# Kernel tuning notes

Hardware: AMD Instinct MI355X
Metric: run time of the kernel (lower is better)

The kernel has to match this reference:

```python
import jax, jax.numpy as jnp
import numpy as np

N_HEAD = 16
N_KV = 4
HEAD_DIM = 64
QK_SCALE = 1.2
VE_GATE_CH = 12


def rms_norm(x):
    # F.rms_norm with default eps = finfo(dtype).eps, no learned scale
    eps = jnp.asarray(jnp.finfo(x.dtype).eps, x.dtype)
    return x * jax.lax.rsqrt(jnp.mean(x * x, axis=-1, keepdims=True) + eps)


def apply_rotary(x, cos, sin):
    # x: (B,T,H,D); cos/sin: (1,T,1,D//2)
    d = x.shape[-1] // 2
    x1, x2 = x[..., :d], x[..., d:]
    return jnp.concatenate([x1 * cos + x2 * sin, -x1 * sin + x2 * cos], axis=-1)


def setup_inputs() -> dict:
    key = jax.random.key(0)
    ks = jax.random.split(key, 8)
    B, T, C = 2, 2048, 1024
    x = jax.random.normal(ks[0], (B, T, C), jnp.float32)
    ve = jax.random.normal(ks[1], (B, T, N_KV * HEAD_DIM), jnp.float32)
    # realistic rotary tables for positions 0..T
    half = HEAD_DIM // 2
    inv_freq = 1.0 / (10000.0 ** (np.arange(half, dtype=np.float64) / half))
    ang = np.arange(T)[:, None] * inv_freq[None, :]
    cos = jnp.asarray(np.cos(ang), jnp.float32)[None, :, None, :]
    sin = jnp.asarray(np.sin(ang), jnp.float32)[None, :, None, :]
    s = 0.02
    Wq = jax.random.normal(ks[2], (N_HEAD * HEAD_DIM, C), jnp.float32) * s
    Wk = jax.random.normal(ks[3], (N_KV * HEAD_DIM, C), jnp.float32) * s
    Wv = jax.random.normal(ks[4], (N_KV * HEAD_DIM, C), jnp.float32) * s
    Wo = jax.random.normal(ks[5], (C, C), jnp.float32) * s
    Wg = jax.random.normal(ks[6], (N_KV, VE_GATE_CH), jnp.float32) * s
    return dict(x=x, ve=ve, cos=cos, sin=sin, Wq=Wq, Wk=Wk, Wv=Wv, Wo=Wo,
                Wg=Wg, window_left=1024)


def reference(x, ve, cos, sin, Wq, Wk, Wv, Wo, Wg, window_left):
    B, T, C = x.shape
    G = N_HEAD // N_KV  # GQA group size
    q = (x @ Wq.T).reshape(B, T, N_HEAD, HEAD_DIM)
    k = (x @ Wk.T).reshape(B, T, N_KV, HEAD_DIM)
    v = (x @ Wv.T).reshape(B, T, N_KV, HEAD_DIM)
    # sigmoid-gated value-embedding mixing
    gate = 3.0 * jax.nn.sigmoid(x[..., :VE_GATE_CH] @ Wg.T)  # (B,T,N_KV)
    v = v + gate[..., None] * ve.reshape(B, T, N_KV, HEAD_DIM)
    # RoPE -> RMSNorm -> qk_scale on both q and k
    q = rms_norm(apply_rotary(q, cos, sin)) * QK_SCALE
    k = rms_norm(apply_rotary(k, cos, sin)) * QK_SCALE
    # GQA attention with causal + sliding window (flash default scale 1/sqrt(d))
    qg = q.reshape(B, T, N_KV, G, HEAD_DIM)
    scale = 1.0 / jnp.sqrt(jnp.asarray(HEAD_DIM, q.dtype))
    scores = jnp.einsum('bqkgd,bskd->bkgqs', qg, k) * scale  # (B,N_KV,G,T,T)
    i = jnp.arange(T)[:, None]
    j = jnp.arange(T)[None, :]
    mask = (j <= i) & (i - j <= window_left)
    scores = jnp.where(mask, scores, jnp.asarray(-1e30, scores.dtype))
    attn = jax.nn.softmax(scores, axis=-1)
    y = jnp.einsum('bkgqs,bskd->bqkgd', attn, v).reshape(B, T, N_HEAD * HEAD_DIM)
    return y @ Wo.T
```

## Files before the change

### kernel.cpp

```cpp
#include <hip/hip_runtime.h>
#include <hip/hip_bf16.h>

#define B_ 2
#define T_ 2048
#define C_ 1024
#define NH 16
#define NKV 4
#define HD 64
#define NQKV 1536
#define KVB 64

typedef __attribute__((ext_vector_type(4))) float f32x4;
typedef __attribute__((ext_vector_type(8))) short bf16x8;
typedef __attribute__((ext_vector_type(4))) short bf16x4;

__device__ __forceinline__ unsigned short f2bf(float f) {
  __hip_bfloat16 h = __float2bfloat16(f);
  unsigned short u;
  __builtin_memcpy(&u, &h, 2);
  return u;
}

__device__ __forceinline__ void gload16(const void* g, void* l) {
  __builtin_amdgcn_global_load_lds(
      (const __attribute__((address_space(1))) void*)g,
      (__attribute__((address_space(3))) void*)l, 16, 0, 0);
}

__device__ __forceinline__ unsigned cvtpk(float lo, float hi_) {
  unsigned w;
  asm("v_cvt_pk_bf16_f32 %0, %1, %2" : "=v"(w) : "v"(lo), "v"(hi_));
  return w;
}

#define NX4  1048576
#define NW4  262144
#define NK4  65536
#define O1 (NX4)
#define O2 (O1 + NW4)
#define O3 (O2 + NK4)
#define O4 (O3 + NK4)
#define OT (O4 + NW4)

__global__ __launch_bounds__(256) void conv_all(
    const float* __restrict__ x, const float* __restrict__ wq, const float* __restrict__ wk,
    const float* __restrict__ wv, const float* __restrict__ wo,
    unsigned short* __restrict__ xb, unsigned short* __restrict__ wqkvb,
    unsigned short* __restrict__ wob) {
  int i = blockIdx.x * blockDim.x + threadIdx.x;
  const int stride = gridDim.x * blockDim.x;
  for (; i < OT; i += stride) {
    const float* src;
    unsigned short* dst;
    int j;
    if (i < O1)      { src = x;  dst = xb;                    j = i; }
    else if (i < O2) { src = wq; dst = wqkvb;                 j = i - O1; }
    else if (i < O3) { src = wk; dst = wqkvb + 1024 * 1024;   j = i - O2; }
    else if (i < O4) { src = wv; dst = wqkvb + 1280 * 1024;   j = i - O3; }
    else             { src = wo; dst = wob;                   j = i - O4; }
    const float4 v = reinterpret_cast<const float4*>(src)[j];
    ushort4 o;
    o.x = f2bf(v.x); o.y = f2bf(v.y); o.z = f2bf(v.z); o.w = f2bf(v.w);
    reinterpret_cast<ushort4*>(dst)[j] = o;
  }
}

#define BK 64

__global__ __launch_bounds__(256) void gemm_qkv(
    const unsigned short* __restrict__ A, const unsigned short* __restrict__ Bw,
    const float* __restrict__ x, const float* __restrict__ ve,
    const float* __restrict__ cosb, const float* __restrict__ sinb,
    const float* __restrict__ Wg,
    unsigned short* __restrict__ Qn, unsigned short* __restrict__ Kn,
    unsigned short* __restrict__ Vt) {
  constexpr int BMT = 128, MI = 4, NI = 2, K = 1024;
  __shared__ char smem[50176];
  unsigned short* AlB = (unsigned short*)smem;
  unsigned short* BlB = (unsigned short*)(smem + 32768);
  const int tid = threadIdx.x;
  const int lane = tid & 63;
  const int wid = tid >> 6;
  const int r = lane & 15, g = lane >> 4;
  const int wm = (wid >> 1) * 64, wn = (wid & 1) * 32;
  const int bm0 = blockIdx.y * BMT, bn0 = blockIdx.x * 64;
  const int lrow = lane >> 3;
  const int lcol = ((lane & 7) ^ lrow) * 8;
  const unsigned short* Asrc = A + (size_t)(bm0 + wid * 32 + lrow) * K + lcol;
  const unsigned short* Bsrc = Bw + (size_t)(bn0 + wid * 16 + lrow) * K + lcol;
  const int fsw = (r & 7) << 4;
  f32x4 acc[MI][NI] = {};

  auto stage = [&](int k0, int buf) {
#pragma unroll
    for (int i = 0; i < 4; ++i)
      gload16(Asrc + (size_t)(i * 8) * K + k0, AlB + buf * 8192 + (wid * 32 + i * 8) * BK);
#pragma unroll
    for (int i = 0; i < 2; ++i)
      gload16(Bsrc + (size_t)(i * 8) * K + k0, BlB + buf * 4096 + (wid * 16 + i * 8) * BK);
  };

  stage(0, 0);
  __syncthreads();
  const int nt = K / BK;
  for (int t = 0; t < nt; ++t) {
    const int cur = t & 1;
    if (t + 1 < nt) stage((t + 1) * BK, cur ^ 1);
    const char* Ac = (const char*)(AlB + cur * 8192);
    const char* Bc = (const char*)(BlB + cur * 4096);
    bf16x8 af[MI][2], bfr[NI][2];
#pragma unroll
    for (int mi = 0; mi < MI; ++mi)
#pragma unroll
      for (int s = 0; s < 2; ++s)
        af[mi][s] = *reinterpret_cast<const bf16x8*>(
            Ac + (wm + mi * 16 + r) * 128 + ((s * 64 + g * 16) ^ fsw));
#pragma unroll
    for (int ni = 0; ni < NI; ++ni)
#pragma unroll
      for (int s = 0; s < 2; ++s)
        bfr[ni][s] = *reinterpret_cast<const bf16x8*>(
            Bc + (wn + ni * 16 + r) * 128 + ((s * 64 + g * 16) ^ fsw));
#pragma unroll
    for (int s = 0; s < 2; ++s)
#pragma unroll
      for (int mi = 0; mi < MI; ++mi)
#pragma unroll
        for (int ni = 0; ni < NI; ++ni)
          acc[mi][ni] = __builtin_amdgcn_mfma_f32_16x16x32_bf16(af[mi][s], bfr[ni][s],
                                                                acc[mi][ni], 0, 0, 0);
    __syncthreads();
  }
  float* Cl = (float*)smem;
  unsigned short* Vst = (unsigned short*)(smem + 33280);
#pragma unroll
  for (int mi = 0; mi < MI; ++mi)
#pragma unroll
    for (int ni = 0; ni < NI; ++ni)
#pragma unroll
      for (int e = 0; e < 4; ++e)
        Cl[(wm + mi * 16 + g * 4 + e) * 65 + wn + ni * 16 + r] = acc[mi][ni][e];
  __syncthreads();
  const int head = blockIdx.x;
  const int trow = tid >> 1, half = tid & 1;
  const int tg = bm0 + trow;
  const int b = tg >> 11, t = tg & 2047;
  if (head < 20) {
    float r1[16], r2[16];
    float sq = 0.f;
#pragma unroll
    for (int i = 0; i < 16; ++i) {
      const int d = half * 16 + i;
      const float x1 = Cl[trow * 65 + d];
      const float x2 = Cl[trow * 65 + d + 32];
      const float c = cosb[t * 32 + d];
      const float s = sinb[t * 32 + d];
      r1[i] = x1 * c + x2 * s;
      r2[i] = x2 * c - x1 * s;
      sq += r1[i] * r1[i] + r2[i] * r2[i];
    }
    sq += __shfl_xor(sq, 1);
    const float sc = rsqrtf(sq * (1.0f / 64.0f) + 1.1920929e-7f) *
                     ((head < 16) ? 0.21640425613334453f : 1.2f);
    unsigned short* dst = (head < 16)
        ? Qn + (((size_t)b * NH + head) * T_ + t) * HD
        : Kn + (((size_t)b * NKV + (head - 16)) * T_ + t) * HD;
#pragma unroll
    for (int i4 = 0; i4 < 4; ++i4) {
      ushort4 w1, w2;
      w1.x = f2bf(r1[i4 * 4 + 0] * sc); w1.y = f2bf(r1[i4 * 4 + 1] * sc);
      w1.z = f2bf(r1[i4 * 4 + 2] * sc); w1.w = f2bf(r1[i4 * 4 + 3] * sc);
      w2.x = f2bf(r2[i4 * 4 + 0] * sc); w2.y = f2bf(r2[i4 * 4 + 1] * sc);
      w2.z = f2bf(r2[i4 * 4 + 2] * sc); w2.w = f2bf(r2[i4 * 4 + 3] * sc);
      *reinterpret_cast<ushort4*>(dst + half * 16 + i4 * 4) = w1;
      *reinterpret_cast<ushort4*>(dst + half * 16 + 32 + i4 * 4) = w2;
    }
  } else {
    const int kv = head - 20;
    float dot = 0.f;
#pragma unroll
    for (int i = 0; i < 12; ++i) dot += x[(size_t)tg * C_ + i] * Wg[kv * 12 + i];
    const float gate = 3.0f / (1.0f + __expf(-dot));
    const float* vsrc = ve + (size_t)tg * (NKV * HD) + kv * HD;
#pragma unroll
    for (int i = 0; i < 32; ++i) {
      const int d = half * 32 + i;
      Vst[d * 128 + trow] = f2bf(Cl[trow * 65 + d] + gate * vsrc[d]);
    }
    __syncthreads();
    const int dd = tid >> 2, t0 = (tid & 3) * 32;
    unsigned short* vd = Vt + (((size_t)b * NKV + kv) * HD + dd) * T_ + (bm0 & 2047) + t0;
    const unsigned short* vs2 = Vst + dd * 128 + t0;
#pragma unroll
    for (int i = 0; i < 4; ++i)
      *reinterpret_cast<bf16x8*>(vd + i * 8) = *reinterpret_cast<const bf16x8*>(vs2 + i * 8);
  }
}

template <int BMT, int BNT, bool OUTBF>
__global__ __launch_bounds__(256) void gemm_bt(const unsigned short* __restrict__ A,
                                               const unsigned short* __restrict__ Bw,
                                               void* __restrict__ Cv, int M, int N, int K) {
  constexpr int MI = BMT / 32;
  constexpr int NI = BNT / 32;
  __shared__ unsigned short Al[2][BMT * BK];
  __shared__ unsigned short Bl[2][BNT * BK];
  const int tid = threadIdx.x;
  const int lane = tid & 63;
  const int wid = tid >> 6;
  const int r = lane & 15, g = lane >> 4;
  const int wm = (wid >> 1) * (BMT / 2), wn = (wid & 1) * (BNT / 2);
  const int bm0 = blockIdx.y * BMT, bn0 = blockIdx.x * BNT;
  const int lrow = lane >> 3;
  const int lcol = ((lane & 7) ^ lrow) * 8;
  const unsigned short* Asrc = A + (size_t)(bm0 + wid * (BMT / 4) + lrow) * K + lcol;
  const unsigned short* Bsrc = Bw + (size_t)(bn0 + wid * (BNT / 4) + lrow) * K + lcol;
  const int fsw = (r & 7) << 4;
  f32x4 acc[MI][NI] = {};

  auto stage = [&](int k0, int buf) {
#pragma unroll
    for (int i = 0; i < BMT / 32; ++i)
      gload16(Asrc + (size_t)(i * 8) * K + k0, Al[buf] + (wid * (BMT / 4) + i * 8) * BK);
#pragma unroll
    for (int i = 0; i < BNT / 32; ++i)
      gload16(Bsrc + (size_t)(i * 8) * K + k0, Bl[buf] + (wid * (BNT / 4) + i * 8) * BK);
  };

  stage(0, 0);
  __syncthreads();
  const int nt = K / BK;
  for (int t = 0; t < nt; ++t) {
    const int cur = t & 1;
    if (t + 1 < nt) stage((t + 1) * BK, cur ^ 1);
    const char* Ac = (const char*)Al[cur];
    const char* Bc = (const char*)Bl[cur];
    bf16x8 af[MI][2], bfr[NI][2];
#pragma unroll
    for (int mi = 0; mi < MI; ++mi)
#pragma unroll
      for (int s = 0; s < 2; ++s)
        af[mi][s] = *reinterpret_cast<const bf16x8*>(
            Ac + (wm + mi * 16 + r) * 128 + ((s * 64 + g * 16) ^ fsw));
#pragma unroll
    for (int ni = 0; ni < NI; ++ni)
#pragma unroll
      for (int s = 0; s < 2; ++s)
        bfr[ni][s] = *reinterpret_cast<const bf16x8*>(
            Bc + (wn + ni * 16 + r) * 128 + ((s * 64 + g * 16) ^ fsw));
#pragma unroll
    for (int s = 0; s < 2; ++s)
#pragma unroll
      for (int mi = 0; mi < MI; ++mi)
#pragma unroll
        for (int ni = 0; ni < NI; ++ni)
          acc[mi][ni] = __builtin_amdgcn_mfma_f32_16x16x32_bf16(af[mi][s], bfr[ni][s],
                                                                acc[mi][ni], 0, 0, 0);
    __syncthreads();
  }
#pragma unroll
  for (int mi = 0; mi < MI; ++mi)
#pragma unroll
    for (int ni = 0; ni < NI; ++ni) {
      const int row = bm0 + wm + mi * 16 + g * 4;
      const int col = bn0 + wn + ni * 16 + r;
#pragma unroll
      for (int e = 0; e < 4; ++e) {
        if (OUTBF)
          ((unsigned short*)Cv)[(size_t)(row + e) * N + col] = f2bf(acc[mi][ni][e]);
        else
          ((float*)Cv)[(size_t)(row + e) * N + col] = acc[mi][ni][e];
      }
    }
}

__global__ __launch_bounds__(256, 4) void attn_fwd(
    const unsigned short* __restrict__ Qn, const unsigned short* __restrict__ Kn,
    const unsigned short* __restrict__ Vt, unsigned short* __restrict__ Y,
    const int* __restrict__ wlp) {
  __shared__ unsigned short Kl[2][KVB * 64];
  __shared__ unsigned short Vl[2][64 * KVB];
  __shared__ unsigned short Pl[4][16 * 64];
  const int flat = blockIdx.x;
  const int kvh = flat & 3, b = (flat >> 2) & 1;
  const int slot = flat >> 3;
  const int h = kvh * 4 + (slot & 3);
  const int j = slot >> 2;
  const int tid = threadIdx.x;
  const int wid = tid >> 6, lane = tid & 63;
  const int r = lane & 15, g = lane >> 4;
  const int wl = *wlp;
  const unsigned short* Kb = Kn + (size_t)(b * NKV + kvh) * T_ * HD;
  const unsigned short* Vb = Vt + (size_t)(b * NKV + kvh) * HD * T_;
  const int lrow = lane >> 3;
  const int lcol = ((lane & 7) ^ lrow) * 8;
  const unsigned short* KsrcG = Kb + (size_t)(wid * 16 + lrow) * HD + lcol;
  const unsigned short* VsrcG = Vb + (size_t)(wid * 16 + lrow) * T_ + lcol;
  char* Pwb = (char*)Pl[wid];
  const int swz = (r & 7) << 4;
  const int ksw = swz;
  const int nseg = (j < 8) ? 2 : 1;

  for (int seg = 0; seg < nseg; ++seg) {
    const int qt = (j < 8) ? (seg ? 15 - j : j) : j + 8;
    const int q0 = qt * 64;
    const int qs = q0 + wid * 16;
    const int q = qs + r;
    const unsigned short* Qb = Qn + ((size_t)(b * NH + h) * T_ + qs) * HD;
    const bf16x8 qf0 = *reinterpret_cast<const bf16x8*>(Qb + r * HD + g * 8);
    const bf16x8 qf1 = *reinterpret_cast<const bf16x8*>(Qb + r * HD + 32 + g * 8);
    float lrun = 0.f;
    f32x4 o[4] = {};
    int slo = q0 - wl; if (slo < 0) slo = 0;
    slo &= ~63;
    const int send = q0 + 63;

    auto stageKV = [&](int sb, int buf) {
#pragma unroll
      for (int i = 0; i < 2; ++i) {
        gload16(KsrcG + (size_t)(sb + i * 8) * HD,
                (unsigned short*)Kl[buf] + (wid * 16 + i * 8) * 64);
        gload16(VsrcG + (size_t)(i * 8) * T_ + sb,
                (unsigned short*)Vl[buf] + (wid * 16 + i * 8) * 64);
      }
    };

    stageKV(slo, 0);
    __syncthreads();

    int cur = 0;
    for (int sb = slo; sb <= send; sb += KVB) {
      const bool has_next = (sb + KVB <= send);
      if (has_next) stageKV(sb + KVB, cur ^ 1);
      {
        const char* Kc = (const char*)Kl[cur];
        const char* Vc = (const char*)Vl[cur];
        float sv[16];
        __builtin_amdgcn_s_setprio(1);
#pragma unroll
        for (int sub = 0; sub < 4; ++sub) {
          const int rowb = (sub * 16 + r) * 128;
          bf16x8 kf0 = *reinterpret_cast<const bf16x8*>(Kc + rowb + ((g * 16) ^ ksw));
          bf16x8 kf1 = *reinterpret_cast<const bf16x8*>(Kc + rowb + ((64 + g * 16) ^ ksw));
          f32x4 z = {};
          z = __builtin_amdgcn_mfma_f32_16x16x32_bf16(kf0, qf0, z, 0, 0, 0);
          z = __builtin_amdgcn_mfma_f32_16x16x32_bf16(kf1, qf1, z, 0, 0, 0);
#pragma unroll
          for (int e = 0; e < 4; ++e) sv[sub * 4 + e] = z[e];
        }
        __builtin_amdgcn_s_setprio(0);
        if (sb + 63 > qs || sb < qs + 15 - wl) {
#pragma unroll
          for (int i = 0; i < 16; ++i) {
            const int s_ = sb + (i >> 2) * 16 + g * 4 + (i & 3);
            const bool ok = (unsigned)(q - s_) <= (unsigned)wl;
            sv[i] = ok ? sv[i] : -__builtin_inff();
          }
        }
        float pe[16];
        float ps = 0.f;
#pragma unroll
        for (int i = 0; i < 16; ++i) {
          pe[i] = __builtin_amdgcn_exp2f(sv[i] - 17.0f);
          ps += pe[i];
        }
        lrun += ps;
#pragma unroll
        for (int sub = 0; sub < 4; ++sub) {
          unsigned w2[2];
          w2[0] = cvtpk(pe[sub * 4 + 0], pe[sub * 4 + 1]);
          w2[1] = cvtpk(pe[sub * 4 + 2], pe[sub * 4 + 3]);
          bf16x4 w;
          __builtin_memcpy(&w, w2, 8);
          *reinterpret_cast<bf16x4*>(Pwb + ((r * 128 + sub * 32 + g * 8) ^ swz)) = w;
        }
        asm volatile("s_waitcnt lgkmcnt(0)" ::: "memory");
        __builtin_amdgcn_s_setprio(1);
#pragma unroll
        for (int c = 0; c < 2; ++c) {
          const bf16x8 pf = *reinterpret_cast<const bf16x8*>(Pwb + ((r * 128 + c * 64 + g * 16) ^ swz));
#pragma unroll
          for (int dt = 0; dt < 4; ++dt) {
            const int vrow = (dt * 16 + r) * 128;
            const bf16x8 vf = *reinterpret_cast<const bf16x8*>(Vc + vrow + ((c * 64 + g * 16) ^ ksw));
            o[dt] = __builtin_amdgcn_mfma_f32_16x16x32_bf16(vf, pf, o[dt], 0, 0, 0);
          }
        }
        __builtin_amdgcn_s_setprio(0);
      }
      __syncthreads();
      cur ^= 1;
    }
    lrun += __shfl_xor(lrun, 16);
    lrun += __shfl_xor(lrun, 32);
    const float inv = 1.0f / lrun;
    unsigned short* Yb = Y + ((size_t)(b * T_) + qs + r) * (NH * HD) + h * HD;
#pragma unroll
    for (int dt = 0; dt < 4; ++dt)
#pragma unroll
      for (int e = 0; e < 4; ++e)
        Yb[dt * 16 + g * 4 + e] = f2bf(o[dt][e] * inv);
  }
}

extern "C" void kernel_launch(void* const* d_in, const int* in_sizes, int n_in,
                              void* d_out, int out_size, void* d_ws, size_t ws_size,
                              hipStream_t stream) {
  const float* x    = (const float*)d_in[0];
  const float* ve   = (const float*)d_in[1];
  const float* cosb = (const float*)d_in[2];
  const float* sinb = (const float*)d_in[3];
  const float* Wq   = (const float*)d_in[4];
  const float* Wk   = (const float*)d_in[5];
  const float* Wv   = (const float*)d_in[6];
  const float* Wo   = (const float*)d_in[7];
  const float* Wg   = (const float*)d_in[8];
  const int*   wlp  = (const int*)d_in[9];

  char* ws = (char*)d_ws;
  unsigned short* xb    = (unsigned short*)ws; ws += (size_t)4096 * 1024 * 2;
  unsigned short* wqkvb = (unsigned short*)ws; ws += (size_t)1536 * 1024 * 2;
  unsigned short* wob   = (unsigned short*)ws; ws += (size_t)1024 * 1024 * 2;
  unsigned short* Qn    = (unsigned short*)ws; ws += (size_t)B_ * NH * T_ * HD * 2;
  unsigned short* Kn    = (unsigned short*)ws; ws += (size_t)B_ * NKV * T_ * HD * 2;
  unsigned short* Vt    = (unsigned short*)ws; ws += (size_t)B_ * NKV * HD * T_ * 2;
  unsigned short* yb    = (unsigned short*)ws; ws += (size_t)4096 * 1024 * 2;

  conv_all<<<dim3(2048), dim3(256), 0, stream>>>(x, Wq, Wk, Wv, Wo, xb, wqkvb, wob);

  gemm_qkv<<<dim3(NQKV / 64, 4096 / 128), dim3(256), 0, stream>>>(
      xb, wqkvb, x, ve, cosb, sinb, Wg, Qn, Kn, Vt);

  attn_fwd<<<dim3(768), dim3(256), 0, stream>>>(Qn, Kn, Vt, yb, wlp);

  gemm_bt<128, 64, false><<<dim3(1024 / 64, 4096 / 128), dim3(256), 0, stream>>>(
      yb, wob, d_out, 4096, 1024, 1024);
}
```

Measured before the change: 76.03 us.

## Load GEMM B operand directly from global into registers, skipping LDS

In both the QKV and output-projection GEMMs, the weight (B) tile is no longer staged through shared memory. Each lane reads its MFMA B fragments straight from global memory into registers, prefetched one k-step ahead. K becomes a compile-time template parameter so the k-loop can be fully unrolled. This removes LDS traffic for B and frees shared memory, but every wave now reloads B fragments from global/L2 itself (B is no longer shared through LDS), which raises global traffic and register pressure.

```diff
diff --git a/kernel.cpp b/kernel.cpp
--- a/kernel.cpp
+++ b/kernel.cpp
@@ -77,7 +77,6 @@
   constexpr int BMT = 128, MI = 4, NI = 2, K = 1024;
   __shared__ char smem[50176];
   unsigned short* AlB = (unsigned short*)smem;
-  unsigned short* BlB = (unsigned short*)(smem + 32768);
   const int tid = threadIdx.x;
   const int lane = tid & 63;
   const int wid = tid >> 6;
@@ -87,28 +86,35 @@
   const int lrow = lane >> 3;
   const int lcol = ((lane & 7) ^ lrow) * 8;
   const unsigned short* Asrc = A + (size_t)(bm0 + wid * 32 + lrow) * K + lcol;
-  const unsigned short* Bsrc = Bw + (size_t)(bn0 + wid * 16 + lrow) * K + lcol;
+  const unsigned short* BsrcD = Bw + (size_t)(bn0 + wn + r) * K + g * 8;
   const int fsw = (r & 7) << 4;
   f32x4 acc[MI][NI] = {};
 
-  auto stage = [&](int k0, int buf) {
+  auto stageA = [&](int k0, int buf) {
 #pragma unroll
     for (int i = 0; i < 4; ++i)
       gload16(Asrc + (size_t)(i * 8) * K + k0, AlB + buf * 8192 + (wid * 32 + i * 8) * BK);
-#pragma unroll
-    for (int i = 0; i < 2; ++i)
-      gload16(Bsrc + (size_t)(i * 8) * K + k0, BlB + buf * 4096 + (wid * 16 + i * 8) * BK);
   };
 
-  stage(0, 0);
+  bf16x8 bcur[NI][2], bnxt[NI][2];
+#define LOADB(DST, K0)                                                          \
+  {                                                                             \
+    _Pragma("unroll") for (int ni = 0; ni < NI; ++ni)                           \
+    _Pragma("unroll") for (int s = 0; s < 2; ++s)                               \
+      DST[ni][s] = *reinterpret_cast<const bf16x8*>(                            \
+          BsrcD + (size_t)(ni * 16) * K + (K0) + s * 32);                       \
+  }
+
+  stageA(0, 0);
+  LOADB(bcur, 0)
   __syncthreads();
-  const int nt = K / BK;
+  constexpr int nt = K / BK;
+#pragma unroll
   for (int t = 0; t < nt; ++t) {
     const int cur = t & 1;
-    if (t + 1 < nt) stage((t + 1) * BK, cur ^ 1);
+    if (t + 1 < nt) { stageA((t + 1) * BK, cur ^ 1); LOADB(bnxt, (t + 1) * BK) }
     const char* Ac = (const char*)(AlB + cur * 8192);
-    const char* Bc = (const char*)(BlB + cur * 4096);
-    bf16x8 af[MI][2], bfr[NI][2];
+    bf16x8 af[MI][2];
 #pragma unroll
     for (int mi = 0; mi < MI; ++mi)
 #pragma unroll
@@ -116,20 +122,20 @@
         af[mi][s] = *reinterpret_cast<const bf16x8*>(
             Ac + (wm + mi * 16 + r) * 128 + ((s * 64 + g * 16) ^ fsw));
 #pragma unroll
-    for (int ni = 0; ni < NI; ++ni)
-#pragma unroll
-      for (int s = 0; s < 2; ++s)
-        bfr[ni][s] = *reinterpret_cast<const bf16x8*>(
-            Bc + (wn + ni * 16 + r) * 128 + ((s * 64 + g * 16) ^ fsw));
-#pragma unroll
     for (int s = 0; s < 2; ++s)
 #pragma unroll
       for (int mi = 0; mi < MI; ++mi)
 #pragma unroll
         for (int ni = 0; ni < NI; ++ni)
-          acc[mi][ni] = __builtin_amdgcn_mfma_f32_16x16x32_bf16(af[mi][s], bfr[ni][s],
+          acc[mi][ni] = __builtin_amdgcn_mfma_f32_16x16x32_bf16(af[mi][s], bcur[ni][s],
                                                                 acc[mi][ni], 0, 0, 0);
     __syncthreads();
+    if (t + 1 < nt) {
+#pragma unroll
+      for (int ni = 0; ni < NI; ++ni)
+#pragma unroll
+        for (int s = 0; s < 2; ++s) bcur[ni][s] = bnxt[ni][s];
+    }
   }
   float* Cl = (float*)smem;
   unsigned short* Vst = (unsigned short*)(smem + 33280);
@@ -197,14 +203,13 @@
   }
 }
 
-template <int BMT, int BNT, bool OUTBF>
+template <int BMT, int BNT, bool OUTBF, int K>
 __global__ __launch_bounds__(256) void gemm_bt(const unsigned short* __restrict__ A,
                                                const unsigned short* __restrict__ Bw,
-                                               void* __restrict__ Cv, int M, int N, int K) {
+                                               void* __restrict__ Cv, int M, int N) {
   constexpr int MI = BMT / 32;
   constexpr int NI = BNT / 32;
   __shared__ unsigned short Al[2][BMT * BK];
-  __shared__ unsigned short Bl[2][BNT * BK];
   const int tid = threadIdx.x;
   const int lane = tid & 63;
   const int wid = tid >> 6;
@@ -214,28 +219,35 @@
   const int lrow = lane >> 3;
   const int lcol = ((lane & 7) ^ lrow) * 8;
   const unsigned short* Asrc = A + (size_t)(bm0 + wid * (BMT / 4) + lrow) * K + lcol;
-  const unsigned short* Bsrc = Bw + (size_t)(bn0 + wid * (BNT / 4) + lrow) * K + lcol;
+  const unsigned short* BsrcD = Bw + (size_t)(bn0 + wn + r) * K + g * 8;
   const int fsw = (r & 7) << 4;
   f32x4 acc[MI][NI] = {};
 
-  auto stage = [&](int k0, int buf) {
+  auto stageA = [&](int k0, int buf) {
 #pragma unroll
     for (int i = 0; i < BMT / 32; ++i)
       gload16(Asrc + (size_t)(i * 8) * K + k0, Al[buf] + (wid * (BMT / 4) + i * 8) * BK);
-#pragma unroll
-    for (int i = 0; i < BNT / 32; ++i)
-      gload16(Bsrc + (size_t)(i * 8) * K + k0, Bl[buf] + (wid * (BNT / 4) + i * 8) * BK);
   };
 
-  stage(0, 0);
+  bf16x8 bcur[NI][2], bnxt[NI][2];
+#define LOADB2(DST, K0)                                                         \
+  {                                                                             \
+    _Pragma("unroll") for (int ni = 0; ni < NI; ++ni)                           \
+    _Pragma("unroll") for (int s = 0; s < 2; ++s)                               \
+      DST[ni][s] = *reinterpret_cast<const bf16x8*>(                            \
+          BsrcD + (size_t)(ni * 16) * K + (K0) + s * 32);                       \
+  }
+
+  stageA(0, 0);
+  LOADB2(bcur, 0)
   __syncthreads();
-  const int nt = K / BK;
+  constexpr int nt = K / BK;
+#pragma unroll
   for (int t = 0; t < nt; ++t) {
     const int cur = t & 1;
-    if (t + 1 < nt) stage((t + 1) * BK, cur ^ 1);
+    if (t + 1 < nt) { stageA((t + 1) * BK, cur ^ 1); LOADB2(bnxt, (t + 1) * BK) }
     const char* Ac = (const char*)Al[cur];
-    const char* Bc = (const char*)Bl[cur];
-    bf16x8 af[MI][2], bfr[NI][2];
+    bf16x8 af[MI][2];
 #pragma unroll
     for (int mi = 0; mi < MI; ++mi)
 #pragma unroll
@@ -243,20 +255,20 @@
         af[mi][s] = *reinterpret_cast<const bf16x8*>(
             Ac + (wm + mi * 16 + r) * 128 + ((s * 64 + g * 16) ^ fsw));
 #pragma unroll
-    for (int ni = 0; ni < NI; ++ni)
-#pragma unroll
-      for (int s = 0; s < 2; ++s)
-        bfr[ni][s] = *reinterpret_cast<const bf16x8*>(
-            Bc + (wn + ni * 16 + r) * 128 + ((s * 64 + g * 16) ^ fsw));
-#pragma unroll
     for (int s = 0; s < 2; ++s)
 #pragma unroll
       for (int mi = 0; mi < MI; ++mi)
 #pragma unroll
         for (int ni = 0; ni < NI; ++ni)
-          acc[mi][ni] = __builtin_amdgcn_mfma_f32_16x16x32_bf16(af[mi][s], bfr[ni][s],
+          acc[mi][ni] = __builtin_amdgcn_mfma_f32_16x16x32_bf16(af[mi][s], bcur[ni][s],
                                                                 acc[mi][ni], 0, 0, 0);
     __syncthreads();
+    if (t + 1 < nt) {
+#pragma unroll
+      for (int ni = 0; ni < NI; ++ni)
+#pragma unroll
+        for (int s = 0; s < 2; ++s) bcur[ni][s] = bnxt[ni][s];
+    }
   }
 #pragma unroll
   for (int mi = 0; mi < MI; ++mi)
@@ -433,6 +445,6 @@
 
   attn_fwd<<<dim3(768), dim3(256), 0, stream>>>(Qn, Kn, Vt, yb, wlp);
 
-  gemm_bt<128, 64, false><<<dim3(1024 / 64, 4096 / 128), dim3(256), 0, stream>>>(
-      yb, wob, d_out, 4096, 1024, 1024);
-}
+  gemm_bt<128, 64, false, 1024><<<dim3(1024 / 64, 4096 / 128), dim3(256), 0, stream>>>(
+      yb, wob, d_out, 4096, 1024);
+}
```

New measurement: 93.56 us. 1.23x slower.
